# Optimization experiments

Measured on AMD Instinct MI355X. Metric: run time of the kernel, lower is better.

The kernel has to match this reference:

```python
import jax, jax.numpy as jnp
import numpy as np

N_NODES = 50000
N_EDGES = 800000
IN_DIM = 128
OUT_DIM = 128
HEADS = 8
C = OUT_DIM // HEADS  # per-head channels = 16
NEG_SLOPE = 0.2
EPS = 1e-16


def setup_inputs() -> dict:
    key = jax.random.key(0)
    k1, k2, k3, k4, k5 = jax.random.split(key, 5)
    x = jax.random.normal(k1, (N_NODES, IN_DIM), dtype=jnp.float32)
    edge_index = jax.random.randint(k2, (2, N_EDGES), 0, N_NODES, dtype=jnp.int32)
    # Glorot-ish scaled params
    W = jax.random.normal(k3, (IN_DIM, HEADS * C), dtype=jnp.float32) * (1.0 / np.sqrt(IN_DIM))
    att_src = jax.random.normal(k4, (HEADS, C), dtype=jnp.float32) * (1.0 / np.sqrt(C))
    att_dst = jax.random.normal(k5, (HEADS, C), dtype=jnp.float32) * (1.0 / np.sqrt(C))
    bias = jnp.zeros((OUT_DIM,), dtype=jnp.float32)
    return {"x": x, "edge_index": edge_index, "W": W, "att_src": att_src, "att_dst": att_dst, "bias": bias}


def _gat_forward(x, edge_index, W, att_src, att_dst, bias):
    N = x.shape[0]
    # PyG GATConv default: add self loops
    loops = jnp.arange(N, dtype=edge_index.dtype)
    ei = jnp.concatenate([edge_index, jnp.stack([loops, loops])], axis=1)  # [2, E+N]
    src, dst = ei[0], ei[1]

    h = (x @ W).reshape(N, HEADS, C)                       # [N, H, C]
    a_src = jnp.einsum('nhc,hc->nh', h, att_src)           # [N, H]
    a_dst = jnp.einsum('nhc,hc->nh', h, att_dst)           # [N, H]

    e = a_src[src] + a_dst[dst]                            # [E, H]
    e = jnp.where(e >= 0, e, NEG_SLOPE * e)                # LeakyReLU(0.2)

    # segment softmax over destination nodes (every node has a self-loop -> non-empty segments)
    emax = jax.ops.segment_max(e, dst, num_segments=N)     # [N, H]
    ex = jnp.exp(e - emax[dst])                            # [E, H]
    denom = jax.ops.segment_sum(ex, dst, num_segments=N)   # [N, H]
    alpha = ex / (denom[dst] + EPS)                        # [E, H]

    msg = h[src] * alpha[:, :, None]                       # [E, H, C]
    out = jax.ops.segment_sum(msg, dst, num_segments=N)    # [N, H, C]
    out = out.reshape(N, HEADS * C) + bias
    return jax.nn.elu(out)


def reference(x, edge_index, W, att_src, att_dst, bias):
    return _gat_forward(x, edge_index, W, att_src, att_dst, bias)
```

## Files before the change

### kernel.cpp

```cpp
#include <hip/hip_runtime.h>
#include <hip/hip_bf16.h>

#define N_NODES 50000
#define N_EDGES 800000
#define HEADS 8
#define DIM 128
#define NEG_SLOPE 0.2f
#define EPS 1e-16f
#define NBUCK 391
#define BCAP 2432
#define BINB 160
#define EPB (N_EDGES / BINB)

__device__ inline unsigned int f2_to_bf2(float a, float b) {
    unsigned int ua = __float_as_uint(a);
    unsigned int ub = __float_as_uint(b);
    ua += 0x7fff + ((ua >> 16) & 1);
    ub += 0x7fff + ((ub >> 16) & 1);
    return (ua >> 16) | (ub & 0xffff0000u);
}
__device__ inline float2 bf2_to_f2(unsigned int u) {
    return make_float2(__uint_as_float(u << 16),
                       __uint_as_float(u & 0xffff0000u));
}

__global__ __launch_bounds__(256) void k_gemm(const float* __restrict__ x,
                                              const float* __restrict__ W,
                                              const float* __restrict__ att_s,
                                              const float* __restrict__ att_d,
                                              unsigned int* __restrict__ h_bf,
                                              float* __restrict__ asrc,
                                              float* __restrict__ adst,
                                              int* __restrict__ cnt) {
    constexpr int LDT = 68;
    __shared__ float xs[128 * LDT];
    const int row0 = blockIdx.x * 64;
    const int tid = threadIdx.x;

    const int gid = blockIdx.x * 256 + tid;
    if (gid < NBUCK) cnt[gid] = 0;

    for (int i = tid; i < 64 * 32; i += 256) {
        const int r = i >> 5;
        const int k4 = i & 31;
        const int row = row0 + r;
        float4 v = make_float4(0.f, 0.f, 0.f, 0.f);
        if (row < N_NODES) v = ((const float4*)x)[row * 32 + k4];
        const int k = k4 * 4;
        xs[(k + 0) * LDT + r] = v.x;
        xs[(k + 1) * LDT + r] = v.y;
        xs[(k + 2) * LDT + r] = v.z;
        xs[(k + 3) * LDT + r] = v.w;
    }
    __syncthreads();

    const int colg = tid & 31;
    const int rowg = tid >> 5;
    float acc[8][4];
#pragma unroll
    for (int r = 0; r < 8; ++r)
#pragma unroll
        for (int j = 0; j < 4; ++j) acc[r][j] = 0.f;

    for (int k = 0; k < 128; ++k) {
        const float4 w = ((const float4*)W)[k * 32 + colg];
        const float* xr = xs + k * LDT + rowg * 8;
        const float4 xa = *(const float4*)(xr);
        const float4 xb = *(const float4*)(xr + 4);
        const float xv[8] = {xa.x, xa.y, xa.z, xa.w, xb.x, xb.y, xb.z, xb.w};
        const float wv[4] = {w.x, w.y, w.z, w.w};
#pragma unroll
        for (int r = 0; r < 8; ++r)
#pragma unroll
            for (int j = 0; j < 4; ++j) acc[r][j] += xv[r] * wv[j];
    }

    const int hd = colg >> 2;
    const float4 asv = ((const float4*)att_s)[colg];
    const float4 adv = ((const float4*)att_d)[colg];
#pragma unroll
    for (int r = 0; r < 8; ++r) {
        const int row = row0 + rowg * 8 + r;
        float ps = acc[r][0] * asv.x + acc[r][1] * asv.y +
                   acc[r][2] * asv.z + acc[r][3] * asv.w;
        float pd = acc[r][0] * adv.x + acc[r][1] * adv.y +
                   acc[r][2] * adv.z + acc[r][3] * adv.w;
        ps += __shfl_xor(ps, 1); ps += __shfl_xor(ps, 2);
        pd += __shfl_xor(pd, 1); pd += __shfl_xor(pd, 2);
        if (row < N_NODES) {
            if ((colg & 3) == 0) {
                asrc[row * 8 + hd] = ps;
                adst[row * 8 + hd] = pd;
            }
            uint2 p;
            p.x = f2_to_bf2(acc[r][0], acc[r][1]);
            p.y = f2_to_bf2(acc[r][2], acc[r][3]);
            ((uint2*)h_bf)[row * 32 + colg] = p;
        }
    }
}

__global__ __launch_bounds__(256) void k_bin(const int* __restrict__ ei,
                                             int* __restrict__ cnt,
                                             unsigned int* __restrict__ bin) {
    __shared__ unsigned int srt[EPB];
    __shared__ int hist[NBUCK];
    __shared__ int base[NBUCK];
    __shared__ int cur[NBUCK];
    __shared__ int gbase[NBUCK];
    __shared__ int sums[128];
    const int tid = threadIdx.x;
    const int e0 = blockIdx.x * EPB;

    for (int b = tid; b < NBUCK; b += 256) hist[b] = 0;
    __syncthreads();

    for (int i = tid; i < EPB; i += 256)
        atomicAdd(&hist[ei[N_EDGES + e0 + i] >> 7], 1);
    __syncthreads();

    int loc0 = 0, loc1 = 0, loc2 = 0, loc3 = 0, tot = 0;
    if (tid < 128) {
        const int b = tid * 4;
        loc0 = (b     < NBUCK) ? hist[b]     : 0;
        loc1 = (b + 1 < NBUCK) ? hist[b + 1] : 0;
        loc2 = (b + 2 < NBUCK) ? hist[b + 2] : 0;
        loc3 = (b + 3 < NBUCK) ? hist[b + 3] : 0;
        tot = loc0 + loc1 + loc2 + loc3;
        sums[tid] = tot;
    }
    __syncthreads();
    for (int off = 1; off < 128; off <<= 1) {
        int v = 0;
        if (tid < 128 && tid >= off) v = sums[tid - off];
        __syncthreads();
        if (tid < 128) sums[tid] += v;
        __syncthreads();
    }
    if (tid < 128) {
        int run = sums[tid] - tot;
        const int b = tid * 4;
        if (b     < NBUCK) { base[b]     = run; cur[b]     = run; } run += loc0;
        if (b + 1 < NBUCK) { base[b + 1] = run; cur[b + 1] = run; } run += loc1;
        if (b + 2 < NBUCK) { base[b + 2] = run; cur[b + 2] = run; } run += loc2;
        if (b + 3 < NBUCK) { base[b + 3] = run; cur[b + 3] = run; }
    }
    __syncthreads();

    for (int i = tid; i < EPB; i += 256) {
        const unsigned src = (unsigned)ei[e0 + i];
        const unsigned dst = (unsigned)ei[N_EDGES + e0 + i];
        const int p = atomicAdd(&cur[dst >> 7], 1);
        if ((unsigned)p < (unsigned)EPB) srt[p] = (dst << 16) | src;
    }
    __syncthreads();

    for (int b = tid; b < NBUCK; b += 256)
        gbase[b] = (hist[b] > 0) ? atomicAdd(&cnt[b], hist[b]) : 0;
    __syncthreads();

    for (int p = tid; p < EPB; p += 256) {
        const unsigned rec = srt[p];
        const int b = rec >> 23;
        if (b < NBUCK) {
            const int pos = gbase[b] + (p - base[b]);
            if ((unsigned)pos < (unsigned)BCAP)
                bin[(size_t)b * BCAP + pos] = rec;
        }
    }
}

__global__ __launch_bounds__(512) void k_aggr(const unsigned int* __restrict__ h_bf,
                                              const unsigned int* __restrict__ bin,
                                              const int* __restrict__ cnt,
                                              const float* __restrict__ asrc,
                                              const float* __restrict__ adst,
                                              const float* __restrict__ bias,
                                              float* __restrict__ out) {
    __shared__ unsigned int srt[BCAP];
    __shared__ int hist[128], base[128], cur[128], scn[128];

    const int bkt = blockIdx.x;
    const int tid = threadIdx.x;
    const int wid = tid >> 6;
    const int lane = tid & 63;
    const int hd = lane >> 3;

    const int cntb = min(cnt[bkt], BCAP);
    const unsigned int* seg = bin + (size_t)bkt * BCAP;

    if (tid < 128) hist[tid] = 0;
    __syncthreads();
    for (int i = tid; i < cntb; i += 512)
        atomicAdd(&hist[(seg[i] >> 16) & 127], 1);
    __syncthreads();
    if (tid < 128) scn[tid] = hist[tid];
    __syncthreads();
    for (int off = 1; off < 128; off <<= 1) {
        int v = 0;
        if (tid < 128 && tid >= off) v = scn[tid - off];
        __syncthreads();
        if (tid < 128) scn[tid] += v;
        __syncthreads();
    }
    if (tid < 128) {
        base[tid] = scn[tid] - hist[tid];
        cur[tid] = base[tid];
    }
    __syncthreads();
    for (int i = tid; i < cntb; i += 512) {
        const unsigned rec = seg[i];
        const int p = atomicAdd(&cur[(rec >> 16) & 127], 1);
        if ((unsigned)p < (unsigned)BCAP) srt[p] = rec;
    }
    __syncthreads();

    for (int dl = wid; dl < 128; dl += 8) {
        const int d = bkt * 128 + dl;
        if (d >= N_NODES) continue;
        const int jb = base[dl];
        const int jn = hist[dl];

        const float adst_h = adst[d * 8 + hd];
        const float asrc_self = asrc[d * 8 + hd];
        const float2 hdv = bf2_to_f2(h_bf[d * 64 + lane]);

        float es = asrc_self + adst_h;
        es = (es >= 0.f) ? es : NEG_SLOPE * es;
        const float exs = __expf(es);

        float2 acc = make_float2(0.f, 0.f);
        float den = 0.f;

        for (int j0 = 0; j0 < jn; j0 += 16) {
            int s[16];
#pragma unroll
            for (int i = 0; i < 16; ++i) {
                const int jj = j0 + i;
                s[i] = (int)(srt[jb + ((jj < jn) ? jj : jn - 1)] & 0xffffu);
            }
            unsigned int hv[16];
            float a[16];
#pragma unroll
            for (int i = 0; i < 16; ++i) {
                hv[i] = h_bf[s[i] * 64 + lane];
                a[i] = asrc[s[i] * 8 + hd];
            }
            const int rem = jn - j0;
#pragma unroll
            for (int i = 0; i < 16; ++i) {
                float e = a[i] + adst_h;
                e = (e >= 0.f) ? e : NEG_SLOPE * e;
                const float ex = (i < rem) ? __expf(e) : 0.f;
                const float2 hv2 = bf2_to_f2(hv[i]);
                acc.x += ex * hv2.x;
                acc.y += ex * hv2.y;
                den += ex;
            }
        }

        const float dtot = den + exs + EPS;
        const float2 b2 = ((const float2*)bias)[lane];
        float vx = (acc.x + exs * hdv.x) / dtot + b2.x;
        float vy = (acc.y + exs * hdv.y) / dtot + b2.y;
        vx = (vx > 0.f) ? vx : expm1f(vx);
        vy = (vy > 0.f) ? vy : expm1f(vy);
        ((float2*)out)[d * 64 + lane] = make_float2(vx, vy);
    }
}

extern "C" void kernel_launch(void* const* d_in, const int* in_sizes, int n_in,
                              void* d_out, int out_size, void* d_ws, size_t ws_size,
                              hipStream_t stream) {
    const float* x     = (const float*)d_in[0];
    const int*   ei    = (const int*)d_in[1];
    const float* W     = (const float*)d_in[2];
    const float* att_s = (const float*)d_in[3];
    const float* att_d = (const float*)d_in[4];
    const float* bias  = (const float*)d_in[5];
    float* out = (float*)d_out;

    unsigned int* h_bf = (unsigned int*)d_ws;
    float* asrc = (float*)(h_bf + (size_t)N_NODES * 64);
    float* adst = asrc + (size_t)N_NODES * HEADS;
    unsigned int* bin = (unsigned int*)(adst + (size_t)N_NODES * HEADS);
    int* cnt = (int*)(bin + (size_t)NBUCK * BCAP);

    k_gemm<<<(N_NODES + 63) / 64, 256, 0, stream>>>(x, W, att_s, att_d,
                                                    h_bf, asrc, adst, cnt);
    k_bin<<<BINB, 256, 0, stream>>>(ei, cnt, bin);
    k_aggr<<<NBUCK, 512, 0, stream>>>(h_bf, bin, cnt, asrc, adst, bias, out);
}
```

Before: 202.5 us.

## Halve aggregation bucket size to 64 nodes and reuse atomic ranks for placement

Destination buckets shrink from 128 to 64 nodes, which doubles the number of aggregation blocks to 782 and lowers the per-block bin capacity, aiming for more parallelism and better load balance. The binning scan now uses all 256 threads. In the aggregation kernel, each thread keeps the rank returned by its histogram atomic in registers and places records with base plus rank, removing the second pass of shared atomics and the global re-read of records. The risk is per-block setup overhead across twice as many blocks, and the register arrays assume at most three records per thread, which holds only while the bucket capacity stays at or below 1536.

```diff
diff --git a/kernel.cpp b/kernel.cpp
--- a/kernel.cpp
+++ b/kernel.cpp
@@ -7,8 +7,9 @@
 #define DIM 128
 #define NEG_SLOPE 0.2f
 #define EPS 1e-16f
-#define NBUCK 391
-#define BCAP 2432
+#define NBUCK 782
+#define BNODES 64
+#define BCAP 1312
 #define BINB 160
 #define EPB (N_EDGES / BINB)
 
@@ -108,7 +109,7 @@
     __shared__ int base[NBUCK];
     __shared__ int cur[NBUCK];
     __shared__ int gbase[NBUCK];
-    __shared__ int sums[128];
+    __shared__ int sums[256];
     const int tid = threadIdx.x;
     const int e0 = blockIdx.x * EPB;
 
@@ -116,11 +117,11 @@
     __syncthreads();
 
     for (int i = tid; i < EPB; i += 256)
-        atomicAdd(&hist[ei[N_EDGES + e0 + i] >> 7], 1);
+        atomicAdd(&hist[ei[N_EDGES + e0 + i] >> 6], 1);
     __syncthreads();
 
     int loc0 = 0, loc1 = 0, loc2 = 0, loc3 = 0, tot = 0;
-    if (tid < 128) {
+    {
         const int b = tid * 4;
         loc0 = (b     < NBUCK) ? hist[b]     : 0;
         loc1 = (b + 1 < NBUCK) ? hist[b + 1] : 0;
@@ -130,14 +131,13 @@
         sums[tid] = tot;
     }
     __syncthreads();
-    for (int off = 1; off < 128; off <<= 1) {
-        int v = 0;
-        if (tid < 128 && tid >= off) v = sums[tid - off];
+    for (int off = 1; off < 256; off <<= 1) {
+        const int v = (tid >= off) ? sums[tid - off] : 0;
         __syncthreads();
-        if (tid < 128) sums[tid] += v;
+        sums[tid] += v;
         __syncthreads();
     }
-    if (tid < 128) {
+    {
         int run = sums[tid] - tot;
         const int b = tid * 4;
         if (b     < NBUCK) { base[b]     = run; cur[b]     = run; } run += loc0;
@@ -150,7 +150,7 @@
     for (int i = tid; i < EPB; i += 256) {
         const unsigned src = (unsigned)ei[e0 + i];
         const unsigned dst = (unsigned)ei[N_EDGES + e0 + i];
-        const int p = atomicAdd(&cur[dst >> 7], 1);
+        const int p = atomicAdd(&cur[dst >> 6], 1);
         if ((unsigned)p < (unsigned)EPB) srt[p] = (dst << 16) | src;
     }
     __syncthreads();
@@ -161,7 +161,7 @@
 
     for (int p = tid; p < EPB; p += 256) {
         const unsigned rec = srt[p];
-        const int b = rec >> 23;
+        const int b = rec >> 22;
         if (b < NBUCK) {
             const int pos = gbase[b] + (p - base[b]);
             if ((unsigned)pos < (unsigned)BCAP)
@@ -178,7 +178,7 @@
                                               const float* __restrict__ bias,
                                               float* __restrict__ out) {
     __shared__ unsigned int srt[BCAP];
-    __shared__ int hist[128], base[128], cur[128], scn[128];
+    __shared__ int hist[BNODES], base[BNODES], scn[BNODES];
 
     const int bkt = blockIdx.x;
     const int tid = threadIdx.x;
@@ -189,34 +189,41 @@
     const int cntb = min(cnt[bkt], BCAP);
     const unsigned int* seg = bin + (size_t)bkt * BCAP;
 
-    if (tid < 128) hist[tid] = 0;
-    __syncthreads();
-    for (int i = tid; i < cntb; i += 512)
-        atomicAdd(&hist[(seg[i] >> 16) & 127], 1);
-    __syncthreads();
-    if (tid < 128) scn[tid] = hist[tid];
-    __syncthreads();
-    for (int off = 1; off < 128; off <<= 1) {
-        int v = 0;
-        if (tid < 128 && tid >= off) v = scn[tid - off];
-        __syncthreads();
-        if (tid < 128) scn[tid] += v;
-        __syncthreads();
-    }
-    if (tid < 128) {
-        base[tid] = scn[tid] - hist[tid];
-        cur[tid] = base[tid];
-    }
-    __syncthreads();
+    if (tid < BNODES) hist[tid] = 0;
+    __syncthreads();
+
+    unsigned int myrec[3];
+    int myrank[3];
+    int nrec = 0;
     for (int i = tid; i < cntb; i += 512) {
         const unsigned rec = seg[i];
-        const int p = atomicAdd(&cur[(rec >> 16) & 127], 1);
+        myrank[nrec] = atomicAdd(&hist[(rec >> 16) & 63], 1);
+        myrec[nrec] = rec;
+        ++nrec;
+    }
+    __syncthreads();
+
+    if (tid < BNODES) scn[tid] = hist[tid];
+    __syncthreads();
+    for (int off = 1; off < BNODES; off <<= 1) {
+        int v = 0;
+        if (tid < BNODES && tid >= off) v = scn[tid - off];
+        __syncthreads();
+        if (tid < BNODES) scn[tid] += v;
+        __syncthreads();
+    }
+    if (tid < BNODES) base[tid] = scn[tid] - hist[tid];
+    __syncthreads();
+
+    for (int k = 0; k < nrec; ++k) {
+        const unsigned rec = myrec[k];
+        const int p = base[(rec >> 16) & 63] + myrank[k];
         if ((unsigned)p < (unsigned)BCAP) srt[p] = rec;
     }
     __syncthreads();
 
-    for (int dl = wid; dl < 128; dl += 8) {
-        const int d = bkt * 128 + dl;
+    for (int dl = wid; dl < BNODES; dl += 8) {
+        const int d = bkt * BNODES + dl;
         if (d >= N_NODES) continue;
         const int jb = base[dl];
         const int jn = hist[dl];
```

Measured after the change: 189.9 us. 6.2% less time.
